# Kernel optimization log

Hardware: AMD Instinct MI355X
Metric: run time of the kernel (lower is better)

## Reference

```python
import jax, jax.numpy as jnp
import numpy as np

DIM = 768
NUM_HEADS = 12
WH, WW = 14, 14
N_TOK = WH * WW + 1  # 197, includes CLS token
NUM_REL_DIST = (2 * WH - 1) * (2 * WW - 1) + 3  # 732
HEAD_DIM = DIM // NUM_HEADS
SCALE = HEAD_DIM ** -0.5


def _relative_position_index():
    # Mirrors the torch buffer construction (constant, int).
    coords = np.stack(np.meshgrid(np.arange(WH), np.arange(WW), indexing='ij'))  # [2,WH,WW]
    cf = coords.reshape(2, -1)  # [2, WH*WW]
    rel = cf[:, :, None] - cf[:, None, :]  # [2, N, N]
    rel = rel.transpose(1, 2, 0).astype(np.int64)
    rel[:, :, 0] += WH - 1
    rel[:, :, 1] += WW - 1
    rel[:, :, 0] *= 2 * WW - 1
    idx = np.zeros((N_TOK, N_TOK), dtype=np.int64)
    idx[1:, 1:] = rel.sum(-1)
    idx[0, 0:] = NUM_REL_DIST - 3
    idx[0:, 0] = NUM_REL_DIST - 2
    idx[0, 0] = NUM_REL_DIST - 1
    return jnp.asarray(idx)

REL_POS_INDEX = _relative_position_index()


def setup_inputs() -> dict:
    key = jax.random.key(0)
    ks = jax.random.split(key, 7)
    B = 64
    x = jax.random.normal(ks[0], (B, N_TOK, DIM), dtype=jnp.float32)
    qkv_weight = jax.random.normal(ks[1], (3 * DIM, DIM), dtype=jnp.float32) * 0.02
    q_bias = jax.random.normal(ks[2], (DIM,), dtype=jnp.float32) * 0.02
    v_bias = jax.random.normal(ks[3], (DIM,), dtype=jnp.float32) * 0.02
    rel_pos_bias_table = jax.random.normal(ks[4], (NUM_REL_DIST, NUM_HEADS), dtype=jnp.float32) * 0.02
    proj_weight = jax.random.normal(ks[5], (DIM, DIM), dtype=jnp.float32) * 0.02
    proj_bias = jax.random.normal(ks[6], (DIM,), dtype=jnp.float32) * 0.02
    return {"x": x, "qkv_weight": qkv_weight, "q_bias": q_bias, "v_bias": v_bias,
            "rel_pos_bias_table": rel_pos_bias_table, "proj_weight": proj_weight,
            "proj_bias": proj_bias}


def reference(x, qkv_weight, q_bias, v_bias, rel_pos_bias_table, proj_weight, proj_bias):
    B, N, C = x.shape
    qkv_bias = jnp.concatenate([q_bias, jnp.zeros_like(v_bias), v_bias])
    qkv = x @ qkv_weight.T + qkv_bias  # [B, N, 3C]
    qkv = qkv.reshape(B, N, 3, NUM_HEADS, HEAD_DIM).transpose(2, 0, 3, 1, 4)
    q, k, v = qkv[0], qkv[1], qkv[2]  # each [B, H, N, D]
    attn = jnp.einsum('bhnd,bhmd->bhnm', q * SCALE, k)  # [B, H, N, N]
    rpb = rel_pos_bias_table[REL_POS_INDEX]  # [N, N, H]
    attn = attn + rpb.transpose(2, 0, 1)[None]  # [1, H, N, N]
    attn = jax.nn.softmax(attn, axis=-1)
    out = jnp.einsum('bhnm,bhmd->bhnd', attn, v)  # [B, H, N, D]
    out = out.transpose(0, 2, 1, 3).reshape(B, N, C)
    return out @ proj_weight.T + proj_bias
```

## Files before the change

### kernel.cpp

```cpp
#include <hip/hip_runtime.h>
#include <hip/hip_bf16.h>

#define DIM 768
#define QKVD 2304
#define NHEADS 12
#define NTOK 197
#define NP 208
#define NPS 232
#define M_ROWS 12608
#define M_PAD 12800
#define HEADS_TOT 768
#define NT 24

typedef __attribute__((ext_vector_type(8))) short bf16x8;
typedef __attribute__((ext_vector_type(4))) float f32x4;

__device__ inline short f2bf(float f) {
  union { __hip_bfloat16 h; short s; } u;
  u.h = __float2bfloat16(f);
  return u.s;
}

__device__ __forceinline__ void gload16(const short* g, short* l) {
  __builtin_amdgcn_global_load_lds((const __attribute__((address_space(1))) void*)g,
                                   (__attribute__((address_space(3))) void*)l, 16, 0, 0);
}

__device__ __forceinline__ int xcd_swz(int orig, int nwg) {
  int q = nwg >> 3, r = nwg & 7;
  int x = orig & 7, p = orig >> 3;
  return (x < r ? x * (q + 1) : r * (q + 1) + (x - r) * q) + p;
}

__global__ void convert_kernel(const float* __restrict__ x, const float* __restrict__ wq,
                               const float* __restrict__ wp,
                               short* __restrict__ xb, short* __restrict__ wqb,
                               short* __restrict__ wpb) {
  int idx = blockIdx.x * 256 + threadIdx.x;
  const int n_x  = M_ROWS * DIM / 4;
  const int n_wq = 3 * DIM * DIM / 4;
  const int n_wp = DIM * DIM / 4;
  const int n_pad = (M_PAD - M_ROWS) * DIM / 4;
  if (idx >= n_x + n_wq + n_wp) {
    int k = idx - n_x - n_wq - n_wp;
    if (k < n_pad) {
      short4 z = {0, 0, 0, 0};
      *(short4*)(xb + (size_t)M_ROWS * DIM + (size_t)k * 4) = z;
    }
    return;
  }
  const float4* src; short* dst; int off;
  if (idx < n_x)             { src = (const float4*)x;  dst = xb;  off = idx; }
  else if (idx < n_x + n_wq) { src = (const float4*)wq; dst = wqb; off = idx - n_x; }
  else                       { src = (const float4*)wp; dst = wpb; off = idx - n_x - n_wq; }
  float4 v = src[off];
  short4 o;
  o.x = f2bf(v.x); o.y = f2bf(v.y); o.z = f2bf(v.z); o.w = f2bf(v.w);
  *(short4*)(dst + (size_t)off * 4) = o;
}

__global__ void rpb_kernel(const float* __restrict__ table, float* __restrict__ rpbf) {
  int idx = blockIdx.x * 256 + threadIdx.x;
  const int tot = NHEADS * NP * NP;
  if (idx >= tot) return;
  int h = idx / (NP * NP);
  int rem = idx - h * NP * NP;
  int i = rem / NP;
  int j = rem - i * NP;
  float v = 0.f;
  if (i < NTOK && j < NTOK) {
    int t;
    if (i == 0 && j == 0) t = 731;
    else if (i == 0)      t = 729;
    else if (j == 0)      t = 730;
    else {
      int p = i - 1, q = j - 1;
      int ri = p / 14, ci = p - ri * 14;
      int rj = q / 14, cj = q - rj * 14;
      t = (ri - rj + 13) * 27 + (ci - cj + 13);
    }
    v = table[t * NHEADS + h];
  }
  rpbf[idx] = v;
}


__device__ __forceinline__ void tile_step(int kt, short* lds,
                                          const short* Asrc, const short* Bsrc, short* sdst,
                                          int aoff, int boff,
                                          bf16x8 (&afc)[8], bf16x8 (&bfc)[4],
                                          bf16x8 (&afn)[8], bf16x8 (&bfn)[4],
                                          f32x4 (&acc)[8][4]) {
  const bool stg = (kt < NT - 3);
  const bool pre = (kt < NT - 1);
  const short* nb = lds + ((kt + 1) & 3) * 16384;
  short* stgd = sdst + ((kt + 3) & 3) * 16384;
  const int kc = (kt + 3) * 32;
  if (stg) { gload16(Asrc + kc, stgd); gload16(Bsrc + kc, stgd + 8192); }
  if (pre) {
#pragma unroll
    for (int n = 0; n < 4; ++n) bfn[n] = *(const bf16x8*)(nb + boff + n * 512);
#pragma unroll
    for (int j = 0; j < 4; ++j) afn[j] = *(const bf16x8*)(nb + aoff + j * 512);
  }
  __builtin_amdgcn_s_setprio(1);
#pragma unroll
  for (int j = 0; j < 4; ++j)
#pragma unroll
    for (int n = 0; n < 4; ++n)
      acc[j][n] = __builtin_amdgcn_mfma_f32_16x16x32_bf16(afc[j], bfc[n], acc[j][n], 0, 0, 0);
  __builtin_amdgcn_s_setprio(0);
  if (stg) { gload16(Asrc + (size_t)128 * DIM + kc, stgd + 4096);
             gload16(Bsrc + (size_t)128 * DIM + kc, stgd + 8192 + 4096); }
  if (pre) {
#pragma unroll
    for (int j = 0; j < 4; ++j) afn[4 + j] = *(const bf16x8*)(nb + aoff + 2048 + j * 512);
  }
  __builtin_amdgcn_s_setprio(1);
#pragma unroll
  for (int j = 0; j < 4; ++j)
#pragma unroll
    for (int n = 0; n < 4; ++n)
      acc[4 + j][n] = __builtin_amdgcn_mfma_f32_16x16x32_bf16(afc[4 + j], bfc[n], acc[4 + j][n], 0, 0, 0);
  __builtin_amdgcn_s_setprio(0);
  if (kt < NT - 3)       { asm volatile("s_waitcnt vmcnt(4)" ::: "memory"); }
  else if (kt == NT - 3) { asm volatile("s_waitcnt vmcnt(0)" ::: "memory"); }
  __builtin_amdgcn_s_barrier();
}

__device__ __forceinline__ void gemm256_mainloop(const short* __restrict__ A,
                                                 const short* __restrict__ Bw,
                                                 int tm, int tn, short* lds, f32x4 (&acc)[8][4]) {
  const int tid = threadIdx.x;
  const int srow = tid >> 2;
  const int sslot = ((tid & 3) - (tid >> 3)) & 3;
  const int l = tid & 63, lr = l & 15, lg = l >> 4;
  const int w = tid >> 6, wm = w >> 2, wn = w & 3;
  const short* Asrc = A + (size_t)(tm * 256 + srow) * DIM + sslot * 8;
  const short* Bsrc = Bw + (size_t)(tn * 256 + srow) * DIM + sslot * 8;
  short* sdst = lds + tid * 8;
  const int slotR = (lg + (lr >> 1)) & 3;
  const int aoff = wm * 4096 + lr * 32 + slotR * 8;
  const int boff = 8192 + (wn >> 1) * 4096 + ((wn & 1) * 64 + lr) * 32 + slotR * 8;
#pragma unroll
  for (int m = 0; m < 8; ++m)
#pragma unroll
    for (int n = 0; n < 4; ++n) { f32x4 z = {0.f, 0.f, 0.f, 0.f}; acc[m][n] = z; }

#pragma unroll
  for (int kt = 0; kt < 3; ++kt) {
    gload16(Asrc + kt * 32, sdst + kt * 16384);
    gload16(Bsrc + kt * 32, sdst + kt * 16384 + 8192);
    gload16(Asrc + (size_t)128 * DIM + kt * 32, sdst + kt * 16384 + 4096);
    gload16(Bsrc + (size_t)128 * DIM + kt * 32, sdst + kt * 16384 + 8192 + 4096);
  }
  asm volatile("s_waitcnt vmcnt(4)" ::: "memory");
  __builtin_amdgcn_s_barrier();

  bf16x8 afA[8], bfA[4], afB[8], bfB[4];
#pragma unroll
  for (int n = 0; n < 4; ++n) bfA[n] = *(const bf16x8*)(lds + boff + n * 512);
#pragma unroll
  for (int j = 0; j < 4; ++j) afA[j] = *(const bf16x8*)(lds + aoff + j * 512);
#pragma unroll
  for (int j = 0; j < 4; ++j) afA[4 + j] = *(const bf16x8*)(lds + aoff + 2048 + j * 512);

  for (int kt = 0; kt < NT; kt += 2) {
    tile_step(kt,     lds, Asrc, Bsrc, sdst, aoff, boff, afA, bfA, afB, bfB, acc);
    tile_step(kt + 1, lds, Asrc, Bsrc, sdst, aoff, boff, afB, bfB, afA, bfA, acc);
  }
}

__global__ __launch_bounds__(512, 2)
void gemm_qkv_kernel(const short* __restrict__ xb, const short* __restrict__ wqb,
                     const float* __restrict__ q_bias, const float* __restrict__ v_bias,
                     short* __restrict__ qkvb) {
  __shared__ __attribute__((aligned(16))) short lds[65536];
  const int wg = xcd_swz(blockIdx.x, 50 * 9);
  const int tn = wg % 9, tm = wg / 9;
  f32x4 acc[8][4];
  gemm256_mainloop(xb, wqb, tm, tn, lds, acc);

  const int tid = threadIdx.x;
  const int w = tid >> 6, wm = w >> 2, wn = w & 3;
  const int l = tid & 63, lr = l & 15, lg = l >> 4;
  const int rbase = tm * 256 + wm * 128, cbase = tn * 256 + wn * 64;
#pragma unroll
  for (int n = 0; n < 4; ++n) {
    int c = cbase + n * 16 + lr;
    int part = (c < 768) ? 0 : ((c < 1536) ? 1 : 2);
    float bias = (part == 0) ? q_bias[c] : ((part == 2) ? v_bias[c - 1536] : 0.f);
    float scl = (part == 0) ? 0.125f : 1.f;
#pragma unroll
    for (int m = 0; m < 8; ++m) {
#pragma unroll
      for (int i = 0; i < 4; ++i) {
        int r = rbase + m * 16 + lg * 4 + i;
        qkvb[(size_t)r * QKVD + c] = f2bf((acc[m][n][i] + bias) * scl);
      }
    }
  }
}

__device__ inline void gemm_tile_mainloop128(const short* __restrict__ A, const short* __restrict__ Bw,
                                             int tm, int tn,
                                             short* As0, short* Bs0, short* As1, short* Bs1,
                                             f32x4 (&acc)[4][4]) {
  const int tid = threadIdx.x;
  const int l = tid & 63, lr = l & 15, lg = l >> 4;
  const int w = tid >> 6, wm = w >> 1, wn = w & 1;
  const int row = tid >> 2;
  const int c8 = (((tid & 3) ^ ((tid >> 3) & 3)) << 3);
  const int rs = (((lg ^ ((lr >> 1) & 3))) << 3);
  const short* Ag = A + (size_t)(tm * 128 + row) * DIM + c8;
  const short* Bg = Bw + (size_t)(tn * 128 + row) * DIM + c8;
  const int dOff = tid * 8;
#pragma unroll
  for (int m = 0; m < 4; ++m)
#pragma unroll
    for (int n = 0; n < 4; ++n) { f32x4 z = {0.f, 0.f, 0.f, 0.f}; acc[m][n] = z; }

  gload16(Ag, As0 + dOff);
  gload16(Ag + (size_t)64 * DIM, As0 + 2048 + dOff);
  gload16(Bg, Bs0 + dOff);
  gload16(Bg + (size_t)64 * DIM, Bs0 + 2048 + dOff);
  __syncthreads();

  for (int kt = 0; kt < NT; ++kt) {
    short* Ac = (kt & 1) ? As1 : As0;
    short* Bc = (kt & 1) ? Bs1 : Bs0;
    short* An = (kt & 1) ? As0 : As1;
    short* Bn = (kt & 1) ? Bs0 : Bs1;
    if (kt < NT - 1) {
      gload16(Ag + (kt + 1) * 32, An + dOff);
      gload16(Ag + (size_t)64 * DIM + (kt + 1) * 32, An + 2048 + dOff);
      gload16(Bg + (kt + 1) * 32, Bn + dOff);
      gload16(Bg + (size_t)64 * DIM + (kt + 1) * 32, Bn + 2048 + dOff);
    }
    bf16x8 af[4], bfr[4];
#pragma unroll
    for (int m = 0; m < 4; ++m)
      af[m] = *(const bf16x8*)(Ac + (wm * 64 + m * 16 + lr) * 32 + rs);
#pragma unroll
    for (int n = 0; n < 4; ++n)
      bfr[n] = *(const bf16x8*)(Bc + (wn * 64 + n * 16 + lr) * 32 + rs);
#pragma unroll
    for (int m = 0; m < 4; ++m)
#pragma unroll
      for (int n = 0; n < 4; ++n)
        acc[m][n] = __builtin_amdgcn_mfma_f32_16x16x32_bf16(af[m], bfr[n], acc[m][n], 0, 0, 0);
    __syncthreads();
  }
}

__global__ __launch_bounds__(512, 1)
void attn_kernel(const short* __restrict__ qkvb, const float* __restrict__ rpbf,
                 short* __restrict__ aout) {
  __shared__ __attribute__((aligned(16))) short Klds[208 * 64];
  __shared__ __attribute__((aligned(16))) short Vlds[64 * NPS];
  __shared__ __attribute__((aligned(16))) short Plds[8 * 16 * NPS];
  const int bh = blockIdx.x;
  const int b = bh / 12, h = bh - b * 12;
  const short* base = qkvb + (size_t)(b * 197) * QKVD;
  const short* Qg = base + h * 64;
  const short* Kg = base + 768 + h * 64;
  const short* Vg = base + 1536 + h * 64;
  const float* RP = rpbf + (size_t)h * NP * NP;
  const int tid = threadIdx.x;
  const int wave = tid >> 6, l = tid & 63, lr = l & 15, lg = l >> 4;

  for (int c = tid; c < 1664; c += 512) {
    int r = c >> 3, sp = c & 7;
    int rr = r < NTOK ? r : NTOK - 1;
    gload16(Kg + (size_t)rr * QKVD + ((sp ^ (r & 7)) << 3), Klds + c * 8);
  }
  for (int idx = tid; idx < 64 * NP; idx += 512) {
    int t = idx >> 6, d = idx & 63;
    int tt = t < NTOK ? t : NTOK - 1;
    Vlds[d * NPS + t] = Vg[(size_t)tt * QKVD + d];
  }
  __syncthreads();
  if (tid < 64) {
    for (int j = NP; j < NPS; ++j) Vlds[tid * NPS + j] = 0;
  }
  __syncthreads();

  short* Pw = Plds + wave * 16 * NPS;
  for (int s = wave; s < 13; s += 8) {
    const int row0 = s * 16;
    const int qrow = (row0 + lr < NTOK) ? (row0 + lr) : (NTOK - 1);
    bf16x8 qf0 = *(const bf16x8*)(Qg + (size_t)qrow * QKVD + lg * 8);
    bf16x8 qf1 = *(const bf16x8*)(Qg + (size_t)qrow * QKVD + 32 + lg * 8);
    f32x4 acc[13];
#pragma unroll
    for (int t = 0; t < 13; ++t) { f32x4 z = {0.f, 0.f, 0.f, 0.f}; acc[t] = z; }
    __builtin_amdgcn_s_setprio(1);
#pragma unroll
    for (int t = 0; t < 13; ++t) {
      int rk = t * 16 + lr;
      int sw = lr & 7;
      bf16x8 kf0 = *(const bf16x8*)(Klds + rk * 64 + ((lg ^ sw) << 3));
      bf16x8 kf1 = *(const bf16x8*)(Klds + rk * 64 + (((4 + lg) ^ sw) << 3));
      acc[t] = __builtin_amdgcn_mfma_f32_16x16x32_bf16(qf0, kf0, acc[t], 0, 0, 0);
      acc[t] = __builtin_amdgcn_mfma_f32_16x16x32_bf16(qf1, kf1, acc[t], 0, 0, 0);
    }
    __builtin_amdgcn_s_setprio(0);
    float sum4[4];
#pragma unroll
    for (int i = 0; i < 4; ++i) {
      const int row = row0 + lg * 4 + i;
      const float* rp = RP + (size_t)row * NP;
      float sv[13];
      float mx = -3e38f;
#pragma unroll
      for (int t = 0; t < 13; ++t) {
        int col = t * 16 + lr;
        float s_ = (col < NTOK) ? (acc[t][i] + rp[col]) : -3e38f;
        sv[t] = s_;
        mx = fmaxf(mx, s_);
      }
      mx = fmaxf(mx, __shfl_xor(mx, 1, 16));
      mx = fmaxf(mx, __shfl_xor(mx, 2, 16));
      mx = fmaxf(mx, __shfl_xor(mx, 4, 16));
      mx = fmaxf(mx, __shfl_xor(mx, 8, 16));
      float sm = 0.f;
#pragma unroll
      for (int t = 0; t < 13; ++t) {
        float p = __expf(sv[t] - mx);
        sm += p;
        Pw[(lg * 4 + i) * NPS + t * 16 + lr] = f2bf(p);
      }
      sm += __shfl_xor(sm, 1, 16);
      sm += __shfl_xor(sm, 2, 16);
      sm += __shfl_xor(sm, 4, 16);
      sm += __shfl_xor(sm, 8, 16);
      sum4[i] = sm;
      Pw[(lg * 4 + i) * NPS + 208 + lr] = 0;
    }
    f32x4 o[4];
#pragma unroll
    for (int dt = 0; dt < 4; ++dt) { f32x4 z = {0.f, 0.f, 0.f, 0.f}; o[dt] = z; }
    __builtin_amdgcn_s_setprio(1);
#pragma unroll
    for (int jb = 0; jb < 7; ++jb) {
      bf16x8 pf = *(const bf16x8*)(Pw + lr * NPS + jb * 32 + lg * 8);
#pragma unroll
      for (int dt = 0; dt < 4; ++dt) {
        bf16x8 vf = *(const bf16x8*)(Vlds + (dt * 16 + lr) * NPS + jb * 32 + lg * 8);
        o[dt] = __builtin_amdgcn_mfma_f32_16x16x32_bf16(pf, vf, o[dt], 0, 0, 0);
      }
    }
    __builtin_amdgcn_s_setprio(0);
#pragma unroll
    for (int i = 0; i < 4; ++i) {
      const int row = row0 + lg * 4 + i;
      if (row < NTOK) {
        float inv = 1.f / sum4[i];
        size_t base2 = (size_t)(b * 197 + row) * DIM + h * 64;
#pragma unroll
        for (int dt = 0; dt < 4; ++dt)
          aout[base2 + dt * 16 + lr] = f2bf(o[dt][i] * inv);
      }
    }
  }
}

__global__ void gemm_proj_kernel(const short* __restrict__ ab, const short* __restrict__ wpb,
                                 const float* __restrict__ proj_bias, float* __restrict__ out) {
  __shared__ __attribute__((aligned(16))) short As0[128 * 32];
  __shared__ __attribute__((aligned(16))) short Bs0[128 * 32];
  __shared__ __attribute__((aligned(16))) short As1[128 * 32];
  __shared__ __attribute__((aligned(16))) short Bs1[128 * 32];
  const int wg = xcd_swz(blockIdx.x, 99 * 6);
  const int tn = wg % 6, tm = wg / 6;
  f32x4 acc[4][4];
  gemm_tile_mainloop128(ab, wpb, tm, tn, As0, Bs0, As1, Bs1, acc);

  const int tid = threadIdx.x;
  const int w = tid >> 6, l = tid & 63, lr = l & 15, lg = l >> 4;
  const int wm = w >> 1, wn = w & 1;
  const int rbase = tm * 128 + wm * 64, cbase = tn * 128 + wn * 64;
#pragma unroll
  for (int n = 0; n < 4; ++n) {
    int c = cbase + n * 16 + lr;
    float pb = proj_bias[c];
#pragma unroll
    for (int m = 0; m < 4; ++m) {
#pragma unroll
      for (int i = 0; i < 4; ++i) {
        int r = rbase + m * 16 + lg * 4 + i;
        if (r < M_ROWS) out[(size_t)r * DIM + c] = acc[m][n][i] + pb;
      }
    }
  }
}

extern "C" void kernel_launch(void* const* d_in, const int* in_sizes, int n_in,
                              void* d_out, int out_size, void* d_ws, size_t ws_size,
                              hipStream_t stream) {
  const float* x         = (const float*)d_in[0];
  const float* wqkv      = (const float*)d_in[1];
  const float* q_bias    = (const float*)d_in[2];
  const float* v_bias    = (const float*)d_in[3];
  const float* table     = (const float*)d_in[4];
  const float* wproj     = (const float*)d_in[5];
  const float* proj_bias = (const float*)d_in[6];
  float* out = (float*)d_out;

  char* p = (char*)d_ws;
  short* xb    = (short*)p; p += (size_t)M_PAD * DIM * 2;
  short* wqb   = (short*)p; p += (size_t)3 * DIM * DIM * 2;
  short* wpb   = (short*)p; p += (size_t)DIM * DIM * 2;
  short* qkvb  = (short*)p; p += (size_t)M_PAD * QKVD * 2;
  float* rpbf  = (float*)p; p += (size_t)NHEADS * NP * NP * 4;
  short* aout  = xb;

  const int conv_tot = (M_ROWS * DIM + 3 * DIM * DIM + DIM * DIM + (M_PAD - M_ROWS) * DIM) / 4;
  convert_kernel<<<(conv_tot + 255) / 256, 256, 0, stream>>>(x, wqkv, wproj, xb, wqb, wpb);
  rpb_kernel<<<(NHEADS * NP * NP + 255) / 256, 256, 0, stream>>>(table, rpbf);
  gemm_qkv_kernel<<<50 * 9, 512, 0, stream>>>(xb, wqb, q_bias, v_bias, qkvb);
  attn_kernel<<<HEADS_TOT, 512, 0, stream>>>(qkvb, rpbf, aout);
  gemm_proj_kernel<<<99 * 6, 256, 0, stream>>>(aout, wpb, proj_bias, out);
}
```

Baseline: 148.4 us.

## Fuse prep kernels, stage GEMM epilogues through LDS, deepen proj pipeline

Merges the bf16 conversion and relative-position-bias expansion into one launch, which removes a kernel launch. The QKV and projection epilogues now go through LDS so that global stores are coalesced 16-byte vectors instead of scattered scalar stores. The projection GEMM drops its double-buffered loop for a 4-stage global_load_lds pipeline with interleaved fragment prefetch and split MFMA phases, mirroring the QKV GEMM. The price is extra LDS round trips and barriers in the epilogues.

Result: faster. 141.6 us (-4.6%).

```diff
diff --git a/kernel.cpp b/kernel.cpp
--- a/kernel.cpp
+++ b/kernel.cpp
@@ -32,39 +32,37 @@
   return (x < r ? x * (q + 1) : r * (q + 1) + (x - r) * q) + p;
 }
 
-__global__ void convert_kernel(const float* __restrict__ x, const float* __restrict__ wq,
-                               const float* __restrict__ wp,
-                               short* __restrict__ xb, short* __restrict__ wqb,
-                               short* __restrict__ wpb) {
+__global__ void prep_kernel(const float* __restrict__ x, const float* __restrict__ wq,
+                            const float* __restrict__ wp, const float* __restrict__ table,
+                            short* __restrict__ xb, short* __restrict__ wqb,
+                            short* __restrict__ wpb, float* __restrict__ rpbf) {
   int idx = blockIdx.x * 256 + threadIdx.x;
   const int n_x  = M_ROWS * DIM / 4;
   const int n_wq = 3 * DIM * DIM / 4;
   const int n_wp = DIM * DIM / 4;
   const int n_pad = (M_PAD - M_ROWS) * DIM / 4;
-  if (idx >= n_x + n_wq + n_wp) {
-    int k = idx - n_x - n_wq - n_wp;
-    if (k < n_pad) {
+  const int conv_tot = n_x + n_wq + n_wp + n_pad;
+  if (idx < conv_tot) {
+    if (idx >= n_x + n_wq + n_wp) {
+      int k = idx - n_x - n_wq - n_wp;
       short4 z = {0, 0, 0, 0};
       *(short4*)(xb + (size_t)M_ROWS * DIM + (size_t)k * 4) = z;
-    }
+      return;
+    }
+    const float4* src; short* dst; int off;
+    if (idx < n_x)             { src = (const float4*)x;  dst = xb;  off = idx; }
+    else if (idx < n_x + n_wq) { src = (const float4*)wq; dst = wqb; off = idx - n_x; }
+    else                       { src = (const float4*)wp; dst = wpb; off = idx - n_x - n_wq; }
+    float4 v = src[off];
+    short4 o;
+    o.x = f2bf(v.x); o.y = f2bf(v.y); o.z = f2bf(v.z); o.w = f2bf(v.w);
+    *(short4*)(dst + (size_t)off * 4) = o;
     return;
   }
-  const float4* src; short* dst; int off;
-  if (idx < n_x)             { src = (const float4*)x;  dst = xb;  off = idx; }
-  else if (idx < n_x + n_wq) { src = (const float4*)wq; dst = wqb; off = idx - n_x; }
-  else                       { src = (const float4*)wp; dst = wpb; off = idx - n_x - n_wq; }
-  float4 v = src[off];
-  short4 o;
-  o.x = f2bf(v.x); o.y = f2bf(v.y); o.z = f2bf(v.z); o.w = f2bf(v.w);
-  *(short4*)(dst + (size_t)off * 4) = o;
-}
-
-__global__ void rpb_kernel(const float* __restrict__ table, float* __restrict__ rpbf) {
-  int idx = blockIdx.x * 256 + threadIdx.x;
-  const int tot = NHEADS * NP * NP;
-  if (idx >= tot) return;
-  int h = idx / (NP * NP);
-  int rem = idx - h * NP * NP;
+  int ridx = idx - conv_tot;
+  if (ridx >= NHEADS * NP * NP) return;
+  int h = ridx / (NP * NP);
+  int rem = ridx - h * NP * NP;
   int i = rem / NP;
   int j = rem - i * NP;
   float v = 0.f;
@@ -81,9 +79,8 @@
     }
     v = table[t * NHEADS + h];
   }
-  rpbf[idx] = v;
-}
-
+  rpbf[ridx] = v;
+}
 
 __device__ __forceinline__ void tile_step(int kt, short* lds,
                                           const short* Asrc, const short* Bsrc, short* sdst,
@@ -184,71 +181,147 @@
   const int tid = threadIdx.x;
   const int w = tid >> 6, wm = w >> 2, wn = w & 3;
   const int l = tid & 63, lr = l & 15, lg = l >> 4;
-  const int rbase = tm * 256 + wm * 128, cbase = tn * 256 + wn * 64;
-#pragma unroll
-  for (int n = 0; n < 4; ++n) {
-    int c = cbase + n * 16 + lr;
-    int part = (c < 768) ? 0 : ((c < 1536) ? 1 : 2);
-    float bias = (part == 0) ? q_bias[c] : ((part == 2) ? v_bias[c - 1536] : 0.f);
-    float scl = (part == 0) ? 0.125f : 1.f;
-#pragma unroll
-    for (int m = 0; m < 8; ++m) {
-#pragma unroll
-      for (int i = 0; i < 4; ++i) {
-        int r = rbase + m * 16 + lg * 4 + i;
-        qkvb[(size_t)r * QKVD + c] = f2bf((acc[m][n][i] + bias) * scl);
-      }
-    }
-  }
-}
-
-__device__ inline void gemm_tile_mainloop128(const short* __restrict__ A, const short* __restrict__ Bw,
-                                             int tm, int tn,
-                                             short* As0, short* Bs0, short* As1, short* Bs1,
+  const int cbase = tn * 256 + wn * 64;
+  for (int half = 0; half < 2; ++half) {
+    if (wm == half) {
+#pragma unroll
+      for (int n = 0; n < 4; ++n) {
+        int c = cbase + n * 16 + lr;
+        int part = (c < 768) ? 0 : ((c < 1536) ? 1 : 2);
+        float bias = (part == 0) ? q_bias[c] : ((part == 2) ? v_bias[c - 1536] : 0.f);
+        float scl = (part == 0) ? 0.125f : 1.f;
+#pragma unroll
+        for (int m = 0; m < 8; ++m)
+#pragma unroll
+          for (int i = 0; i < 4; ++i)
+            lds[(m * 16 + lg * 4 + i) * 264 + wn * 64 + n * 16 + lr] =
+                f2bf((acc[m][n][i] + bias) * scl);
+      }
+    }
+    __syncthreads();
+#pragma unroll
+    for (int p = 0; p < 8; ++p) {
+      int chunk = tid + p * 512;
+      int row = chunk >> 5, ch = chunk & 31;
+      bf16x8 v = *(const bf16x8*)(lds + row * 264 + ch * 8);
+      *(bf16x8*)(qkvb + (size_t)(tm * 256 + half * 128 + row) * QKVD + tn * 256 + ch * 8) = v;
+    }
+    __syncthreads();
+  }
+}
+
+__device__ __forceinline__ void tile_step128(int kt, short* lds,
+                                             const short* Asrc, const short* Bsrc, short* sdst,
+                                             int aoff, int boff,
+                                             bf16x8 (&afc)[4], bf16x8 (&bfc)[4],
+                                             bf16x8 (&afn)[4], bf16x8 (&bfn)[4],
                                              f32x4 (&acc)[4][4]) {
+  const bool stg = (kt < NT - 3);
+  const bool pre = (kt < NT - 1);
+  const short* nb = lds + ((kt + 1) & 3) * 8192;
+  short* stgd = sdst + ((kt + 3) & 3) * 8192;
+  const int kc = (kt + 3) * 32;
+  if (stg) { gload16(Asrc + kc, stgd); gload16(Bsrc + kc, stgd + 4096); }
+  if (pre) {
+#pragma unroll
+    for (int n = 0; n < 4; ++n) bfn[n] = *(const bf16x8*)(nb + boff + n * 512);
+#pragma unroll
+    for (int j = 0; j < 2; ++j) afn[j] = *(const bf16x8*)(nb + aoff + j * 512);
+  }
+  __builtin_amdgcn_s_setprio(1);
+#pragma unroll
+  for (int j = 0; j < 2; ++j)
+#pragma unroll
+    for (int n = 0; n < 4; ++n)
+      acc[j][n] = __builtin_amdgcn_mfma_f32_16x16x32_bf16(afc[j], bfc[n], acc[j][n], 0, 0, 0);
+  __builtin_amdgcn_s_setprio(0);
+  if (stg) { gload16(Asrc + (size_t)64 * DIM + kc, stgd + 2048);
+             gload16(Bsrc + (size_t)64 * DIM + kc, stgd + 4096 + 2048); }
+  if (pre) {
+#pragma unroll
+    for (int j = 2; j < 4; ++j) afn[j] = *(const bf16x8*)(nb + aoff + j * 512);
+  }
+  __builtin_amdgcn_s_setprio(1);
+#pragma unroll
+  for (int j = 2; j < 4; ++j)
+#pragma unroll
+    for (int n = 0; n < 4; ++n)
+      acc[j][n] = __builtin_amdgcn_mfma_f32_16x16x32_bf16(afc[j], bfc[n], acc[j][n], 0, 0, 0);
+  __builtin_amdgcn_s_setprio(0);
+  if (kt < NT - 3)       { asm volatile("s_waitcnt vmcnt(4)" ::: "memory"); }
+  else if (kt == NT - 3) { asm volatile("s_waitcnt vmcnt(0)" ::: "memory"); }
+  __builtin_amdgcn_s_barrier();
+}
+
+__global__ __launch_bounds__(256, 2)
+void gemm_proj_kernel(const short* __restrict__ ab, const short* __restrict__ wpb,
+                      const float* __restrict__ proj_bias, float* __restrict__ out) {
+  __shared__ __attribute__((aligned(16))) short lds[32768];
+  const int wg = xcd_swz(blockIdx.x, 99 * 6);
+  const int tn = wg % 6, tm = wg / 6;
   const int tid = threadIdx.x;
+  const int srow = tid >> 2;
+  const int sslot = ((tid & 3) - (tid >> 3)) & 3;
   const int l = tid & 63, lr = l & 15, lg = l >> 4;
   const int w = tid >> 6, wm = w >> 1, wn = w & 1;
-  const int row = tid >> 2;
-  const int c8 = (((tid & 3) ^ ((tid >> 3) & 3)) << 3);
-  const int rs = (((lg ^ ((lr >> 1) & 3))) << 3);
-  const short* Ag = A + (size_t)(tm * 128 + row) * DIM + c8;
-  const short* Bg = Bw + (size_t)(tn * 128 + row) * DIM + c8;
-  const int dOff = tid * 8;
+  const short* Asrc = ab + (size_t)(tm * 128 + srow) * DIM + sslot * 8;
+  const short* Bsrc = wpb + (size_t)(tn * 128 + srow) * DIM + sslot * 8;
+  short* sdst = lds + tid * 8;
+  const int slotR = (lg + (lr >> 1)) & 3;
+  const int aoff = wm * 2048 + lr * 32 + slotR * 8;
+  const int boff = 4096 + wn * 2048 + lr * 32 + slotR * 8;
+  f32x4 acc[4][4];
 #pragma unroll
   for (int m = 0; m < 4; ++m)
 #pragma unroll
     for (int n = 0; n < 4; ++n) { f32x4 z = {0.f, 0.f, 0.f, 0.f}; acc[m][n] = z; }
 
-  gload16(Ag, As0 + dOff);
-  gload16(Ag + (size_t)64 * DIM, As0 + 2048 + dOff);
-  gload16(Bg, Bs0 + dOff);
-  gload16(Bg + (size_t)64 * DIM, Bs0 + 2048 + dOff);
-  __syncthreads();
-
-  for (int kt = 0; kt < NT; ++kt) {
-    short* Ac = (kt & 1) ? As1 : As0;
-    short* Bc = (kt & 1) ? Bs1 : Bs0;
-    short* An = (kt & 1) ? As0 : As1;
-    short* Bn = (kt & 1) ? Bs0 : Bs1;
-    if (kt < NT - 1) {
-      gload16(Ag + (kt + 1) * 32, An + dOff);
-      gload16(Ag + (size_t)64 * DIM + (kt + 1) * 32, An + 2048 + dOff);
-      gload16(Bg + (kt + 1) * 32, Bn + dOff);
-      gload16(Bg + (size_t)64 * DIM + (kt + 1) * 32, Bn + 2048 + dOff);
-    }
-    bf16x8 af[4], bfr[4];
-#pragma unroll
-    for (int m = 0; m < 4; ++m)
-      af[m] = *(const bf16x8*)(Ac + (wm * 64 + m * 16 + lr) * 32 + rs);
-#pragma unroll
-    for (int n = 0; n < 4; ++n)
-      bfr[n] = *(const bf16x8*)(Bc + (wn * 64 + n * 16 + lr) * 32 + rs);
-#pragma unroll
-    for (int m = 0; m < 4; ++m)
-#pragma unroll
-      for (int n = 0; n < 4; ++n)
-        acc[m][n] = __builtin_amdgcn_mfma_f32_16x16x32_bf16(af[m], bfr[n], acc[m][n], 0, 0, 0);
+#pragma unroll
+  for (int kt = 0; kt < 3; ++kt) {
+    gload16(Asrc + kt * 32, sdst + kt * 8192);
+    gload16(Bsrc + kt * 32, sdst + kt * 8192 + 4096);
+    gload16(Asrc + (size_t)64 * DIM + kt * 32, sdst + kt * 8192 + 2048);
+    gload16(Bsrc + (size_t)64 * DIM + kt * 32, sdst + kt * 8192 + 4096 + 2048);
+  }
+  asm volatile("s_waitcnt vmcnt(4)" ::: "memory");
+  __builtin_amdgcn_s_barrier();
+
+  bf16x8 afA[4], bfA[4], afB[4], bfB[4];
+#pragma unroll
+  for (int n = 0; n < 4; ++n) bfA[n] = *(const bf16x8*)(lds + boff + n * 512);
+#pragma unroll
+  for (int j = 0; j < 4; ++j) afA[j] = *(const bf16x8*)(lds + aoff + j * 512);
+
+  for (int kt = 0; kt < NT; kt += 2) {
+    tile_step128(kt,     lds, Asrc, Bsrc, sdst, aoff, boff, afA, bfA, afB, bfB, acc);
+    tile_step128(kt + 1, lds, Asrc, Bsrc, sdst, aoff, boff, afB, bfB, afA, bfA, acc);
+  }
+
+  float* ldsF = (float*)lds;
+  for (int half = 0; half < 2; ++half) {
+    if (wm == half) {
+#pragma unroll
+      for (int n = 0; n < 4; ++n) {
+        int c = tn * 128 + wn * 64 + n * 16 + lr;
+        float pb = proj_bias[c];
+#pragma unroll
+        for (int m = 0; m < 4; ++m)
+#pragma unroll
+          for (int i = 0; i < 4; ++i)
+            ldsF[(m * 16 + lg * 4 + i) * 132 + wn * 64 + n * 16 + lr] = acc[m][n][i] + pb;
+      }
+    }
+    __syncthreads();
+#pragma unroll
+    for (int p = 0; p < 8; ++p) {
+      int chunk = tid + p * 256;
+      int row = chunk >> 5, ch = chunk & 31;
+      int r = tm * 128 + half * 64 + row;
+      if (r < M_ROWS) {
+        f32x4 v = *(const f32x4*)(ldsF + row * 132 + ch * 4);
+        *(f32x4*)(out + (size_t)r * DIM + tn * 128 + ch * 4) = v;
+      }
+    }
     __syncthreads();
   }
 }
@@ -365,36 +438,6 @@
   }
 }
 
-__global__ void gemm_proj_kernel(const short* __restrict__ ab, const short* __restrict__ wpb,
-                                 const float* __restrict__ proj_bias, float* __restrict__ out) {
-  __shared__ __attribute__((aligned(16))) short As0[128 * 32];
-  __shared__ __attribute__((aligned(16))) short Bs0[128 * 32];
-  __shared__ __attribute__((aligned(16))) short As1[128 * 32];
-  __shared__ __attribute__((aligned(16))) short Bs1[128 * 32];
-  const int wg = xcd_swz(blockIdx.x, 99 * 6);
-  const int tn = wg % 6, tm = wg / 6;
-  f32x4 acc[4][4];
-  gemm_tile_mainloop128(ab, wpb, tm, tn, As0, Bs0, As1, Bs1, acc);
-
-  const int tid = threadIdx.x;
-  const int w = tid >> 6, l = tid & 63, lr = l & 15, lg = l >> 4;
-  const int wm = w >> 1, wn = w & 1;
-  const int rbase = tm * 128 + wm * 64, cbase = tn * 128 + wn * 64;
-#pragma unroll
-  for (int n = 0; n < 4; ++n) {
-    int c = cbase + n * 16 + lr;
-    float pb = proj_bias[c];
-#pragma unroll
-    for (int m = 0; m < 4; ++m) {
-#pragma unroll
-      for (int i = 0; i < 4; ++i) {
-        int r = rbase + m * 16 + lg * 4 + i;
-        if (r < M_ROWS) out[(size_t)r * DIM + c] = acc[m][n][i] + pb;
-      }
-    }
-  }
-}
-
 extern "C" void kernel_launch(void* const* d_in, const int* in_sizes, int n_in,
                               void* d_out, int out_size, void* d_ws, size_t ws_size,
                               hipStream_t stream) {
@@ -416,8 +459,8 @@
   short* aout  = xb;
 
   const int conv_tot = (M_ROWS * DIM + 3 * DIM * DIM + DIM * DIM + (M_PAD - M_ROWS) * DIM) / 4;
-  convert_kernel<<<(conv_tot + 255) / 256, 256, 0, stream>>>(x, wqkv, wproj, xb, wqb, wpb);
-  rpb_kernel<<<(NHEADS * NP * NP + 255) / 256, 256, 0, stream>>>(table, rpbf);
+  const int prep_tot = conv_tot + NHEADS * NP * NP;
+  prep_kernel<<<(prep_tot + 255) / 256, 256, 0, stream>>>(x, wqkv, wproj, table, xb, wqb, wpb, rpbf);
   gemm_qkv_kernel<<<50 * 9, 512, 0, stream>>>(xb, wqb, q_bias, v_bias, qkvb);
   attn_kernel<<<HEADS_TOT, 512, 0, stream>>>(qkvb, rpbf, aout);
   gemm_proj_kernel<<<99 * 6, 256, 0, stream>>>(aout, wpb, proj_bias, out);
```
